# Kernel optimization log

Measured on AMD Instinct MI355X. Metric: run time of the kernel, lower is better.

Reference implementation:

```python
import jax, jax.numpy as jnp
import numpy as np

N_NODES = 100000
N_EDGES = 1600000
D_IN = 128
D_OUT = 256


def setup_inputs() -> dict:
    key = jax.random.key(0)
    k1, k2, k3 = jax.random.split(key, 3)
    H = jax.random.normal(k1, (N_NODES, D_IN), dtype=jnp.float32)
    edge_index = jax.random.randint(k2, (2, N_EDGES), 0, N_NODES, dtype=jnp.int64)
    # kaiming_normal_ on (in, out): fan computed over dim 1 -> std = sqrt(2/out)
    W = jax.random.normal(k3, (D_IN, D_OUT), dtype=jnp.float32) * np.sqrt(2.0 / D_OUT)
    return {"H": H, "edge_index": edge_index, "W": W}


def reference(H, edge_index, W):
    src, dst = edge_index[0], edge_index[1]
    # gather source node features per edge, scatter-add into destination nodes
    msgs = H[src]  # [E, D_IN]
    new_H = jax.ops.segment_sum(msgs, dst, num_segments=H.shape[0])  # [N, D_IN]
    out = H + new_H
    out = out @ W  # [N, D_OUT]
    return jax.nn.relu(out)
```

## Files before the change

### kernel.cpp

```cpp
#include <hip/hip_runtime.h>

#define N_NODES 100000
#define N_EDGES 1600000
#define D_IN    128
#define D_OUT   256
#define NB_SCAN ((N_NODES + 255) / 256)
#define BLK_ROWS 64
#define N_TILES  ((N_NODES + BLK_ROWS - 1) / BLK_ROWS)
#define X_ROWS   (N_TILES * BLK_ROWS)

#define NBUCK      98
#define BCAP       20480
#define BIN_CHUNK  1024
#define BIN_BLOCKS ((N_EDGES + BIN_CHUNK - 1) / BIN_CHUNK)

typedef __attribute__((ext_vector_type(8))) short short8v;
typedef __attribute__((ext_vector_type(4))) float f32x4;

__device__ __forceinline__ unsigned bf16_rn(float f) {
    unsigned u = __float_as_uint(f);
    return (u + 0x7FFFu + ((u >> 16) & 1u)) >> 16;
}
__device__ __forceinline__ unsigned pack2_bf16(float a, float b) {
    return bf16_rn(a) | (bf16_rn(b) << 16);
}

__global__ void detect_idx64_kernel(const int* __restrict__ edge32,
                                    int* __restrict__ flag,
                                    int* __restrict__ balloc) {
    const int t = threadIdx.x;
    if (t < 128) balloc[t] = 0;
    if (t == 0 && blockIdx.x == 0) {
        int is64 = 1;
        for (int i = 1; i < 32; i += 2) {
            if (edge32[i] != 0) { is64 = 0; break; }
        }
        *flag = is64;
    }
}

__device__ __forceinline__ int load_dst(const void* edge_raw, int is64, int e) {
    if (is64) return (int)((const long long*)edge_raw)[(long long)N_EDGES + e];
    return ((const int*)edge_raw)[N_EDGES + e];
}
__device__ __forceinline__ int load_src(const void* edge_raw, int is64, int e) {
    if (is64) return (int)((const long long*)edge_raw)[e];
    return ((const int*)edge_raw)[e];
}

__global__ __launch_bounds__(256) void cvt_h_kernel(
        const float* __restrict__ H, unsigned* __restrict__ Hb) {
    int i = blockIdx.x * 256 + threadIdx.x;
    if (i >= N_NODES * (D_IN / 2)) return;
    const float2 h = ((const float2*)H)[i];
    Hb[i] = pack2_bf16(h.x, h.y);
}

__global__ __launch_bounds__(256) void pack_w_kernel(
        const float* __restrict__ W, unsigned short* __restrict__ Wp) {
    int t = blockIdx.x * 256 + threadIdx.x;
    if (t >= 64 * 64) return;
    const int f  = t >> 6;
    const int l  = t & 63;
    const int nb = f >> 2;
    const int ks = f & 3;
    const int col  = nb * 16 + (l & 15);
    const int krow = ks * 32 + (l >> 4) * 8;
    #pragma unroll
    for (int i = 0; i < 8; ++i)
        Wp[(size_t)t * 8 + i] = (unsigned short)bf16_rn(W[(krow + i) * D_OUT + col]);
}

__global__ __launch_bounds__(256) void bin_hist_kernel(
        const void* __restrict__ edge_raw, const int* __restrict__ flag,
        int* __restrict__ bucket_alloc, int* __restrict__ binned) {
    __shared__ int cnt[128];
    __shared__ int gbase[128];
    const int tid = threadIdx.x;
    if (tid < 128) cnt[tid] = 0;
    __syncthreads();
    const int is64 = *flag;
    const int base = blockIdx.x * BIN_CHUNK + tid;

#define EDGE_A(i)                                                             \
    int rec##i = 0, pb##i = -1;                                               \
    {                                                                         \
        const int idx = base + (i) * 256;                                     \
        if (idx < N_EDGES) {                                                  \
            const int s = load_src(edge_raw, is64, idx);                      \
            const int d = load_dst(edge_raw, is64, idx);                      \
            if ((unsigned)s < N_NODES && (unsigned)d < N_NODES) {             \
                const int b = d >> 10;                                        \
                const int pos = atomicAdd(&cnt[b], 1);                        \
                rec##i = s | ((d & 1023) << 17);                              \
                pb##i  = pos | (b << 12);                                     \
            }                                                                 \
        }                                                                     \
    }
    EDGE_A(0) EDGE_A(1) EDGE_A(2) EDGE_A(3)
#undef EDGE_A

    __syncthreads();
    if (tid < NBUCK) gbase[tid] = atomicAdd(&bucket_alloc[tid], cnt[tid]);
    __syncthreads();

#define EDGE_B(i)                                                             \
    if (pb##i >= 0) {                                                         \
        const int b = pb##i >> 12;                                            \
        const int p = gbase[b] + (pb##i & 4095);                              \
        if (p < BCAP) binned[b * BCAP + p] = rec##i;                          \
    }
    EDGE_B(0) EDGE_B(1) EDGE_B(2) EDGE_B(3)
#undef EDGE_B
}

__global__ __launch_bounds__(1024) void bucket_fill_scan_kernel(
        const int* __restrict__ bucket_alloc,
        const int* __restrict__ binned,
        int* __restrict__ row_start, int* __restrict__ csr_pack) {
    __shared__ int hist[1024];
    __shared__ int sb[128];
    const int b   = blockIdx.x;
    const int tid = threadIdx.x;
    hist[tid] = 0;
    if (tid < 128) sb[tid] = (tid < NBUCK) ? bucket_alloc[tid] : 0;
    __syncthreads();

    for (int off = 1; off < 128; off <<= 1) {
        const int u = (tid >= off && tid < 128) ? sb[tid - off] : 0;
        __syncthreads();
        if (tid < 128) sb[tid] += u;
        __syncthreads();
    }
    int cnt = bucket_alloc[b];
    const int segb = sb[b] - cnt;
    if (cnt > BCAP) cnt = BCAP;
    const int base = b * BCAP;

    for (int p = tid; p < cnt; p += 1024)
        atomicAdd(&hist[(binned[base + p] >> 17) & 1023], 1);
    __syncthreads();

    const int myc = hist[tid];
    for (int off = 1; off < 1024; off <<= 1) {
        const int u = (tid >= off) ? hist[tid - off] : 0;
        __syncthreads();
        hist[tid] += u;
        __syncthreads();
    }
    const int rs = segb + hist[tid] - myc;
    const int node = (b << 10) + tid;
    if (node <= N_NODES) row_start[node] = rs;

    hist[tid] = rs;
    __syncthreads();

    for (int p = tid; p < cnt; p += 1024) {
        const int rec = binned[base + p];
        const int dlo = (rec >> 17) & 1023;
        const int pos = atomicAdd(&hist[dlo], 1);
        csr_pack[pos] = (rec & 0x1FFFF) | ((dlo & 63) << 20);
    }
}

__global__ __launch_bounds__(256) void gather_mfma_kernel(
        const float* __restrict__ H,
        const unsigned* __restrict__ Hb,
        const int* __restrict__ row_start,
        const int* __restrict__ csr_pack,
        const unsigned short* __restrict__ Wp,
        float* __restrict__ out) {
    __shared__ unsigned Xs[64 * 64];
    __shared__ int idx_lds[4][256];

    const int g    = blockIdx.x * BLK_ROWS;
    const int wv   = threadIdx.x >> 6;
    const int lane = threadIdx.x & 63;
    const int r0   = g + wv * 16;

    if (r0 < N_NODES) {
        int r1 = r0 + 16; if (r1 > N_NODES) r1 = N_NODES;
        const int p0   = row_start[r0];
        const int pend = row_start[r1];

        for (int r = r0; r < r1; ++r) {
            if (row_start[r + 1] == row_start[r]) {
                const float2 h = ((const float2*)(H + (size_t)r * D_IN))[lane];
                const int rr = r - g;
                Xs[rr * 64 + ((((lane >> 2) ^ (rr & 7)) << 2) | (lane & 3))] =
                    pack2_bf16(h.x, h.y);
            }
        }

        int    cur = -1;
        float2 acc = make_float2(0.f, 0.f);
        float2 hs  = make_float2(0.f, 0.f);

#define FLUSH()                                                               \
        Xs[cur * 64 + ((((lane >> 2) ^ (cur & 7)) << 2) | (lane & 3))] =      \
            pack2_bf16(acc.x + hs.x, acc.y + hs.y);

#define PROC(EV, UU)                                                          \
        {                                                                     \
            const int dl = (EV) >> 20;                                        \
            const float vx = __uint_as_float((UU) << 16);                     \
            const float vy = __uint_as_float((UU) & 0xFFFF0000u);             \
            if (dl != cur) {                                                  \
                if (cur >= 0) { FLUSH(); }                                    \
                cur = dl;                                                     \
                hs  = ((const float2*)(H + (size_t)(g + dl) * D_IN))[lane];   \
                acc = make_float2(vx, vy);                                    \
            } else {                                                          \
                acc.x += vx; acc.y += vy;                                     \
            }                                                                 \
        }

        for (int p = p0; p < pend; p += 256) {
            int m = pend - p;
            if (m > 256) m = 256;
            #pragma unroll
            for (int j = 0; j < 4; ++j) {
                const int o = lane + j * 64;
                if (o < m) idx_lds[wv][o] = csr_pack[p + o];
            }
            int n = 0;
            for (; n + 8 <= m; n += 8) {
                const int e0 = idx_lds[wv][n + 0];
                const int e1 = idx_lds[wv][n + 1];
                const int e2 = idx_lds[wv][n + 2];
                const int e3 = idx_lds[wv][n + 3];
                const int e4 = idx_lds[wv][n + 4];
                const int e5 = idx_lds[wv][n + 5];
                const int e6 = idx_lds[wv][n + 6];
                const int e7 = idx_lds[wv][n + 7];
                const unsigned u0 = Hb[(size_t)(e0 & 0xFFFFF) * 64 + lane];
                const unsigned u1 = Hb[(size_t)(e1 & 0xFFFFF) * 64 + lane];
                const unsigned u2 = Hb[(size_t)(e2 & 0xFFFFF) * 64 + lane];
                const unsigned u3 = Hb[(size_t)(e3 & 0xFFFFF) * 64 + lane];
                const unsigned u4 = Hb[(size_t)(e4 & 0xFFFFF) * 64 + lane];
                const unsigned u5 = Hb[(size_t)(e5 & 0xFFFFF) * 64 + lane];
                const unsigned u6 = Hb[(size_t)(e6 & 0xFFFFF) * 64 + lane];
                const unsigned u7 = Hb[(size_t)(e7 & 0xFFFFF) * 64 + lane];
                PROC(e0, u0) PROC(e1, u1) PROC(e2, u2) PROC(e3, u3)
                PROC(e4, u4) PROC(e5, u5) PROC(e6, u6) PROC(e7, u7)
            }
            for (; n < m; ++n) {
                const int e0 = idx_lds[wv][n];
                const unsigned u = Hb[(size_t)(e0 & 0xFFFFF) * 64 + lane];
                PROC(e0, u)
            }
        }
        if (cur >= 0) { FLUSH(); }
#undef PROC
#undef FLUSH
    }
    __syncthreads();

    f32x4 acc4[4][4] = {};
    const int arow = lane & 15;
    const int agrp = lane >> 4;

    #pragma unroll
    for (int ks = 0; ks < 4; ++ks) {
        short8v a0, a1, a2, a3;
        {
            const int r = 0 * 16 + arow;
            a0 = *(const short8v*)(&Xs[r * 64 + ((ks * 4 + agrp) ^ (r & 7)) * 4]);
        }
        {
            const int r = 1 * 16 + arow;
            a1 = *(const short8v*)(&Xs[r * 64 + ((ks * 4 + agrp) ^ (r & 7)) * 4]);
        }
        {
            const int r = 2 * 16 + arow;
            a2 = *(const short8v*)(&Xs[r * 64 + ((ks * 4 + agrp) ^ (r & 7)) * 4]);
        }
        {
            const int r = 3 * 16 + arow;
            a3 = *(const short8v*)(&Xs[r * 64 + ((ks * 4 + agrp) ^ (r & 7)) * 4]);
        }
        #pragma unroll
        for (int nb = 0; nb < 4; ++nb) {
            const int f = (wv * 4 + nb) * 4 + ks;
            const short8v bf = *(const short8v*)(Wp + ((size_t)f * 64 + lane) * 8);
            acc4[0][nb] = __builtin_amdgcn_mfma_f32_16x16x32_bf16(a0, bf, acc4[0][nb], 0, 0, 0);
            acc4[1][nb] = __builtin_amdgcn_mfma_f32_16x16x32_bf16(a1, bf, acc4[1][nb], 0, 0, 0);
            acc4[2][nb] = __builtin_amdgcn_mfma_f32_16x16x32_bf16(a2, bf, acc4[2][nb], 0, 0, 0);
            acc4[3][nb] = __builtin_amdgcn_mfma_f32_16x16x32_bf16(a3, bf, acc4[3][nb], 0, 0, 0);
        }
    }

    #pragma unroll
    for (int mg = 0; mg < 4; ++mg) {
        #pragma unroll
        for (int rr = 0; rr < 4; ++rr) {
            const int row = g + mg * 16 + agrp * 4 + rr;
            if (row < N_NODES) {
                #pragma unroll
                for (int nb = 0; nb < 4; ++nb) {
                    const float v = acc4[mg][nb][rr];
                    out[(size_t)row * D_OUT + wv * 64 + nb * 16 + (lane & 15)] =
                        fmaxf(v, 0.f);
                }
            }
        }
    }
}

__global__ __launch_bounds__(256) void hist_kernel(
        const void* __restrict__ edge_raw, const int* __restrict__ flag,
        int* __restrict__ counts) {
    int e = blockIdx.x * blockDim.x + threadIdx.x;
    if (e >= N_EDGES) return;
    int dst = load_dst(edge_raw, *flag, e);
    if ((unsigned)dst < N_NODES) atomicAdd(&counts[dst], 1);
}

__global__ __launch_bounds__(256) void block_sum_kernel(
        const int* __restrict__ counts, int* __restrict__ bsum) {
    __shared__ int lds[256];
    int t = threadIdx.x;
    int i = blockIdx.x * 256 + t;
    lds[t] = (i < N_NODES) ? counts[i] : 0;
    __syncthreads();
    for (int off = 128; off > 0; off >>= 1) {
        if (t < off) lds[t] += lds[t + off];
        __syncthreads();
    }
    if (t == 0) bsum[blockIdx.x] = lds[0];
}

__global__ __launch_bounds__(512) void scan_bsum_kernel(
        int* __restrict__ bsum, int* __restrict__ row_start) {
    __shared__ int lds[512];
    int t = threadIdx.x;
    lds[t] = (t < NB_SCAN) ? bsum[t] : 0;
    __syncthreads();
    for (int off = 1; off < 512; off <<= 1) {
        int u = (t >= off) ? lds[t - off] : 0;
        __syncthreads();
        lds[t] += u;
        __syncthreads();
    }
    int excl = (t == 0) ? 0 : lds[t - 1];
    if (t < NB_SCAN) bsum[t] = excl;
    if (t == 0) row_start[N_NODES] = N_EDGES;
}

__global__ __launch_bounds__(256) void scan_counts_kernel(
        int* __restrict__ counts_cursor, const int* __restrict__ bsum,
        int* __restrict__ row_start) {
    __shared__ int lds[256];
    int t = threadIdx.x;
    int i = blockIdx.x * 256 + t;
    int c = (i < N_NODES) ? counts_cursor[i] : 0;
    lds[t] = c;
    __syncthreads();
    for (int off = 1; off < 256; off <<= 1) {
        int u = (t >= off) ? lds[t - off] : 0;
        __syncthreads();
        lds[t] += u;
        __syncthreads();
    }
    int rs = bsum[blockIdx.x] + lds[t] - c;
    if (i < N_NODES) {
        row_start[i] = rs;
        counts_cursor[i] = rs;
    }
}

__global__ __launch_bounds__(256) void fill_kernel(
        const void* __restrict__ edge_raw, const int* __restrict__ flag,
        int* __restrict__ cursor, int* __restrict__ csr_pack) {
    int e = blockIdx.x * blockDim.x + threadIdx.x;
    if (e >= N_EDGES) return;
    int is64 = *flag;
    int src = load_src(edge_raw, is64, e);
    int dst = load_dst(edge_raw, is64, e);
    if ((unsigned)dst >= N_NODES || (unsigned)src >= N_NODES) return;
    int pos = atomicAdd(&cursor[dst], 1);
    csr_pack[pos] = src | ((dst & 63) << 20);
}

__global__ __launch_bounds__(256) void fused_gather_gemm_relu_kernel(
        const float* __restrict__ H,
        const int* __restrict__ row_start,
        const int* __restrict__ csr_pack,
        const float* __restrict__ Wm,
        float* __restrict__ out) {
    __shared__ float Xs[BLK_ROWS][D_IN];
    __shared__ int idx_lds[4][64];

    const int g    = blockIdx.x * BLK_ROWS;
    const int tid  = threadIdx.x;
    const int wv   = tid >> 6;
    const int lane = tid & 63;

    {
        const int kidx = tid & 31;
        const int rg   = tid >> 5;
        #pragma unroll
        for (int j = 0; j < 8; ++j) {
            const int r = rg + j * 8;
            const int row = g + r;
            float4 x = make_float4(0.f, 0.f, 0.f, 0.f);
            if (row < N_NODES)
                x = *reinterpret_cast<const float4*>(H + (size_t)row * D_IN + kidx * 4);
            *reinterpret_cast<float4*>(&Xs[r][kidx * 4]) = x;
        }
    }
    __syncthreads();

    {
        const int seg_beg = row_start[g];
        const int rend    = (g + BLK_ROWS < N_NODES) ? (g + BLK_ROWS) : N_NODES;
        const int seg_end = row_start[rend];
        const int len     = seg_end - seg_beg;
        const int clen    = (len + 3) >> 2;
        const int cbeg    = seg_beg + wv * clen;
        int cend          = cbeg + clen;
        if (cend > seg_end) cend = seg_end;

        const int c2 = lane * 2;
        int   cur = -1;
        float2 acc = make_float2(0.f, 0.f);

#define PROCF(EV, VV)                                                         \
        {                                                                     \
            const int dl = (EV) >> 20;                                        \
            if (dl != cur) {                                                  \
                if (cur >= 0) {                                               \
                    atomicAdd(&Xs[cur][c2],     acc.x);                       \
                    atomicAdd(&Xs[cur][c2 + 1], acc.y);                       \
                }                                                             \
                cur = dl;                                                     \
                acc = (VV);                                                   \
            } else {                                                          \
                acc.x += (VV).x; acc.y += (VV).y;                             \
            }                                                                 \
        }

        for (int base = cbeg; base < cend; base += 64) {
            int m = cend - base;
            if (m > 64) m = 64;
            if (lane < m) idx_lds[wv][lane] = csr_pack[base + lane];
            int n = 0;
            for (; n + 8 <= m; n += 8) {
                const int e0 = idx_lds[wv][n + 0];
                const int e1 = idx_lds[wv][n + 1];
                const int e2 = idx_lds[wv][n + 2];
                const int e3 = idx_lds[wv][n + 3];
                const int e4 = idx_lds[wv][n + 4];
                const int e5 = idx_lds[wv][n + 5];
                const int e6 = idx_lds[wv][n + 6];
                const int e7 = idx_lds[wv][n + 7];
                const float2 v0 = ((const float2*)(H + (size_t)(e0 & 0xFFFFF) * D_IN))[lane];
                const float2 v1 = ((const float2*)(H + (size_t)(e1 & 0xFFFFF) * D_IN))[lane];
                const float2 v2 = ((const float2*)(H + (size_t)(e2 & 0xFFFFF) * D_IN))[lane];
                const float2 v3 = ((const float2*)(H + (size_t)(e3 & 0xFFFFF) * D_IN))[lane];
                const float2 v4 = ((const float2*)(H + (size_t)(e4 & 0xFFFFF) * D_IN))[lane];
                const float2 v5 = ((const float2*)(H + (size_t)(e5 & 0xFFFFF) * D_IN))[lane];
                const float2 v6 = ((const float2*)(H + (size_t)(e6 & 0xFFFFF) * D_IN))[lane];
                const float2 v7 = ((const float2*)(H + (size_t)(e7 & 0xFFFFF) * D_IN))[lane];
                PROCF(e0, v0) PROCF(e1, v1) PROCF(e2, v2) PROCF(e3, v3)
                PROCF(e4, v4) PROCF(e5, v5) PROCF(e6, v6) PROCF(e7, v7)
            }
            for (; n < m; ++n) {
                const int e0 = idx_lds[wv][n];
                const float2 v = ((const float2*)(H + (size_t)(e0 & 0xFFFFF) * D_IN))[lane];
                PROCF(e0, v)
            }
        }
        if (cur >= 0) {
            atomicAdd(&Xs[cur][c2],     acc.x);
            atomicAdd(&Xs[cur][c2 + 1], acc.y);
        }
#undef PROCF
    }
    __syncthreads();

    const int ty = tid >> 6;
    const int tx = tid & 63;

    float accv[16][4];
    #pragma unroll
    for (int r = 0; r < 16; ++r)
        #pragma unroll
        for (int j = 0; j < 4; ++j) accv[r][j] = 0.f;

    const float* Wp2 = Wm + tx * 4;

    #pragma unroll 2
    for (int k = 0; k < D_IN; k += 4) {
        const float4 w0 = *reinterpret_cast<const float4*>(Wp2 + (k + 0) * D_OUT);
        const float4 w1 = *reinterpret_cast<const float4*>(Wp2 + (k + 1) * D_OUT);
        const float4 w2 = *reinterpret_cast<const float4*>(Wp2 + (k + 2) * D_OUT);
        const float4 w3 = *reinterpret_cast<const float4*>(Wp2 + (k + 3) * D_OUT);
        #pragma unroll
        for (int r = 0; r < 16; ++r) {
            const float4 x = *reinterpret_cast<const float4*>(&Xs[ty * 16 + r][k]);
            accv[r][0] = fmaf(x.x, w0.x, accv[r][0]);
            accv[r][0] = fmaf(x.y, w1.x, accv[r][0]);
            accv[r][0] = fmaf(x.z, w2.x, accv[r][0]);
            accv[r][0] = fmaf(x.w, w3.x, accv[r][0]);
            accv[r][1] = fmaf(x.x, w0.y, accv[r][1]);
            accv[r][1] = fmaf(x.y, w1.y, accv[r][1]);
            accv[r][1] = fmaf(x.z, w2.y, accv[r][1]);
            accv[r][1] = fmaf(x.w, w3.y, accv[r][1]);
            accv[r][2] = fmaf(x.x, w0.z, accv[r][2]);
            accv[r][2] = fmaf(x.y, w1.z, accv[r][2]);
            accv[r][2] = fmaf(x.z, w2.z, accv[r][2]);
            accv[r][2] = fmaf(x.w, w3.z, accv[r][2]);
            accv[r][3] = fmaf(x.x, w0.w, accv[r][3]);
            accv[r][3] = fmaf(x.y, w1.w, accv[r][3]);
            accv[r][3] = fmaf(x.z, w2.w, accv[r][3]);
            accv[r][3] = fmaf(x.w, w3.w, accv[r][3]);
        }
    }

    #pragma unroll
    for (int r = 0; r < 16; ++r) {
        const int row = g + ty * 16 + r;
        if (row < N_NODES) {
            float4 o;
            o.x = fmaxf(accv[r][0], 0.f);
            o.y = fmaxf(accv[r][1], 0.f);
            o.z = fmaxf(accv[r][2], 0.f);
            o.w = fmaxf(accv[r][3], 0.f);
            *reinterpret_cast<float4*>(out + (size_t)row * D_OUT + tx * 4) = o;
        }
    }
}

extern "C" void kernel_launch(void* const* d_in, const int* in_sizes, int n_in,
                              void* d_out, int out_size, void* d_ws, size_t ws_size,
                              hipStream_t stream) {
    const float* H    = (const float*)d_in[0];
    const void*  edge = d_in[1];
    const float* Wm   = (const float*)d_in[2];
    float* out = (float*)d_out;

    const size_t off_rs    = 0;
    const size_t off_cur   = ((size_t)(N_NODES + 1) * 4 + 15) & ~(size_t)15;
    const size_t off_alloc = off_cur + (size_t)N_NODES * 4;
    const size_t off_csr   = off_alloc + 512;
    const size_t off_bsum  = off_csr + (size_t)N_EDGES * 4;
    const size_t off_flag  = off_bsum + (((size_t)NB_SCAN * 4 + 15) & ~(size_t)15);
    const size_t off_wp    = (off_flag + 16 + 255) & ~(size_t)255;
    const size_t off_X     = (off_wp + 64 * 64 * 16 + 255) & ~(size_t)255;
    const size_t need_mid  = off_X + (size_t)X_ROWS * 64 * sizeof(unsigned);
    const size_t off_Hb    = (need_mid + 255) & ~(size_t)255;
    const size_t need_full = off_Hb + (size_t)N_NODES * (D_IN / 2) * sizeof(unsigned);
    const size_t off_bin   = (need_full + 255) & ~(size_t)255;
    const size_t need_sort = off_bin + (size_t)NBUCK * BCAP * 4;

    int* row_start = (int*)((char*)d_ws + off_rs);
    int* cursor    = (int*)((char*)d_ws + off_cur);
    int* balloc    = (int*)((char*)d_ws + off_alloc);
    int* csr_pack  = (int*)((char*)d_ws + off_csr);
    int* bsum      = (int*)((char*)d_ws + off_bsum);
    int* flag      = (int*)((char*)d_ws + off_flag);
    unsigned short* Wp = (unsigned short*)((char*)d_ws + off_wp);
    unsigned* Hb   = (unsigned*)((char*)d_ws + off_Hb);
    int* binned    = (int*)((char*)d_ws + off_bin);

    detect_idx64_kernel<<<1, 128, 0, stream>>>((const int*)edge, flag, balloc);

    const int edge_blocks = (N_EDGES + 255) / 256;

    if (ws_size >= need_sort) {
        pack_w_kernel<<<16, 256, 0, stream>>>(Wm, Wp);
        cvt_h_kernel<<<(N_NODES * (D_IN / 2) + 255) / 256, 256, 0, stream>>>(H, Hb);
        bin_hist_kernel<<<BIN_BLOCKS, 256, 0, stream>>>(edge, flag, balloc, binned);
        bucket_fill_scan_kernel<<<NBUCK, 1024, 0, stream>>>(
            balloc, binned, row_start, csr_pack);
        gather_mfma_kernel<<<N_TILES, 256, 0, stream>>>(
            H, Hb, row_start, csr_pack, Wp, out);
    } else {
        hipMemsetAsync(cursor, 0, (size_t)N_NODES * 4 + 512, stream);
        hist_kernel<<<edge_blocks, 256, 0, stream>>>(edge, flag, cursor);
        block_sum_kernel<<<NB_SCAN, 256, 0, stream>>>(cursor, bsum);
        scan_bsum_kernel<<<1, 512, 0, stream>>>(bsum, row_start);
        scan_counts_kernel<<<NB_SCAN, 256, 0, stream>>>(cursor, bsum, row_start);
        fill_kernel<<<edge_blocks, 256, 0, stream>>>(edge, flag, cursor, csr_pack);
        fused_gather_gemm_relu_kernel<<<N_TILES, 256, 0, stream>>>(
            H, row_start, csr_pack, Wm, out);
    }
}
```

Baseline: 206.3 us.

## Merge prep kernels and split gather from MFMA GEMM via bf16 buffer

Three preprocessing kernels (W packing, H bf16 conversion, edge binning) are merged into one launch dispatched by block index. The fused gather+GEMM kernel is split into a gather kernel with 32-row blocks (8 rows per wave) that writes bf16 aggregated rows to a global buffer with nontemporal stores. A separate GEMM kernel then loads 64-row tiles into swizzled LDS and preloads the W fragments into registers. This raises parallelism for the irregular gather and separates it from the MFMA phase, at the cost of an extra global round-trip of about 25 MB and one more kernel launch.

```diff
diff --git a/kernel.cpp b/kernel.cpp
--- a/kernel.cpp
+++ b/kernel.cpp
@@ -13,6 +13,11 @@
 #define BCAP       20480
 #define BIN_CHUNK  1024
 #define BIN_BLOCKS ((N_EDGES + BIN_CHUNK - 1) / BIN_CHUNK)
+#define CVT_BLOCKS ((N_NODES * (D_IN / 2) + 255) / 256)
+#define PACK_BLOCKS 16
+
+#define GBLK_ROWS  32
+#define G_TILES    ((N_NODES + GBLK_ROWS - 1) / GBLK_ROWS)
 
 typedef __attribute__((ext_vector_type(8))) short short8v;
 typedef __attribute__((ext_vector_type(4))) float f32x4;
@@ -48,39 +53,43 @@
     return ((const int*)edge_raw)[e];
 }
 
-__global__ __launch_bounds__(256) void cvt_h_kernel(
-        const float* __restrict__ H, unsigned* __restrict__ Hb) {
-    int i = blockIdx.x * 256 + threadIdx.x;
-    if (i >= N_NODES * (D_IN / 2)) return;
-    const float2 h = ((const float2*)H)[i];
-    Hb[i] = pack2_bf16(h.x, h.y);
-}
-
-__global__ __launch_bounds__(256) void pack_w_kernel(
-        const float* __restrict__ W, unsigned short* __restrict__ Wp) {
-    int t = blockIdx.x * 256 + threadIdx.x;
-    if (t >= 64 * 64) return;
-    const int f  = t >> 6;
-    const int l  = t & 63;
-    const int nb = f >> 2;
-    const int ks = f & 3;
-    const int col  = nb * 16 + (l & 15);
-    const int krow = ks * 32 + (l >> 4) * 8;
-    #pragma unroll
-    for (int i = 0; i < 8; ++i)
-        Wp[(size_t)t * 8 + i] = (unsigned short)bf16_rn(W[(krow + i) * D_OUT + col]);
-}
-
-__global__ __launch_bounds__(256) void bin_hist_kernel(
+__global__ __launch_bounds__(256) void prep_kernel(
+        const float* __restrict__ W, unsigned short* __restrict__ Wp,
+        const float* __restrict__ H, unsigned* __restrict__ Hb,
         const void* __restrict__ edge_raw, const int* __restrict__ flag,
         int* __restrict__ bucket_alloc, int* __restrict__ binned) {
+    const int blk = blockIdx.x;
+    const int tid = threadIdx.x;
+
+    if (blk < PACK_BLOCKS) {
+        const int t = blk * 256 + tid;
+        const int f  = t >> 6;
+        const int l  = t & 63;
+        const int nb = f >> 2;
+        const int ks = f & 3;
+        const int col  = nb * 16 + (l & 15);
+        const int krow = ks * 32 + (l >> 4) * 8;
+        #pragma unroll
+        for (int i = 0; i < 8; ++i)
+            Wp[(size_t)t * 8 + i] =
+                (unsigned short)bf16_rn(W[(krow + i) * D_OUT + col]);
+        return;
+    }
+    if (blk < PACK_BLOCKS + CVT_BLOCKS) {
+        const int i = (blk - PACK_BLOCKS) * 256 + tid;
+        if (i < N_NODES * (D_IN / 2)) {
+            const float2 h = ((const float2*)H)[i];
+            Hb[i] = pack2_bf16(h.x, h.y);
+        }
+        return;
+    }
+
     __shared__ int cnt[128];
     __shared__ int gbase[128];
-    const int tid = threadIdx.x;
     if (tid < 128) cnt[tid] = 0;
     __syncthreads();
     const int is64 = *flag;
-    const int base = blockIdx.x * BIN_CHUNK + tid;
+    const int base = (blk - PACK_BLOCKS - CVT_BLOCKS) * BIN_CHUNK + tid;
 
 #define EDGE_A(i)                                                             \
     int rec##i = 0, pb##i = -1;                                               \
@@ -163,102 +172,131 @@
     }
 }
 
-__global__ __launch_bounds__(256) void gather_mfma_kernel(
+__global__ __launch_bounds__(256) void gather_bf16_kernel(
         const float* __restrict__ H,
         const unsigned* __restrict__ Hb,
         const int* __restrict__ row_start,
         const int* __restrict__ csr_pack,
+        unsigned* __restrict__ Xg) {
+    __shared__ int idx_lds[4][256];
+
+    const int gb   = blockIdx.x * GBLK_ROWS;
+    const int tile = (gb >> 6) << 6;
+    const int wv   = threadIdx.x >> 6;
+    const int lane = threadIdx.x & 63;
+    const int r0   = gb + wv * 8;
+    if (r0 >= N_NODES) return;
+    int r1 = r0 + 8; if (r1 > N_NODES) r1 = N_NODES;
+
+    const int p0   = row_start[r0];
+    const int pend = row_start[r1];
+
+    for (int r = r0; r < r1; ++r) {
+        if (row_start[r + 1] == row_start[r]) {
+            const float2 h = ((const float2*)(H + (size_t)r * D_IN))[lane];
+            __builtin_nontemporal_store(pack2_bf16(h.x, h.y),
+                                        &Xg[(size_t)r * 64 + lane]);
+        }
+    }
+
+    int    cur = -1;
+    float2 acc = make_float2(0.f, 0.f);
+    float2 hs  = make_float2(0.f, 0.f);
+
+#define FLUSH()                                                               \
+    __builtin_nontemporal_store(pack2_bf16(acc.x + hs.x, acc.y + hs.y),       \
+                                &Xg[(size_t)(tile + cur) * 64 + lane]);
+
+#define PROC(EV, UU)                                                          \
+    {                                                                         \
+        const int dl = (EV) >> 20;                                            \
+        const float vx = __uint_as_float((UU) << 16);                         \
+        const float vy = __uint_as_float((UU) & 0xFFFF0000u);                 \
+        if (dl != cur) {                                                      \
+            if (cur >= 0) { FLUSH(); }                                        \
+            cur = dl;                                                         \
+            hs  = ((const float2*)(H + (size_t)(tile + dl) * D_IN))[lane];    \
+            acc = make_float2(vx, vy);                                        \
+        } else {                                                              \
+            acc.x += vx; acc.y += vy;                                         \
+        }                                                                     \
+    }
+
+    for (int p = p0; p < pend; p += 256) {
+        int m = pend - p;
+        if (m > 256) m = 256;
+        #pragma unroll
+        for (int j = 0; j < 4; ++j) {
+            const int o = lane + j * 64;
+            if (o < m) idx_lds[wv][o] = csr_pack[p + o];
+        }
+        int n = 0;
+        for (; n + 8 <= m; n += 8) {
+            const int e0 = idx_lds[wv][n + 0];
+            const int e1 = idx_lds[wv][n + 1];
+            const int e2 = idx_lds[wv][n + 2];
+            const int e3 = idx_lds[wv][n + 3];
+            const int e4 = idx_lds[wv][n + 4];
+            const int e5 = idx_lds[wv][n + 5];
+            const int e6 = idx_lds[wv][n + 6];
+            const int e7 = idx_lds[wv][n + 7];
+            const unsigned u0 = Hb[(size_t)(e0 & 0xFFFFF) * 64 + lane];
+            const unsigned u1 = Hb[(size_t)(e1 & 0xFFFFF) * 64 + lane];
+            const unsigned u2 = Hb[(size_t)(e2 & 0xFFFFF) * 64 + lane];
+            const unsigned u3 = Hb[(size_t)(e3 & 0xFFFFF) * 64 + lane];
+            const unsigned u4 = Hb[(size_t)(e4 & 0xFFFFF) * 64 + lane];
+            const unsigned u5 = Hb[(size_t)(e5 & 0xFFFFF) * 64 + lane];
+            const unsigned u6 = Hb[(size_t)(e6 & 0xFFFFF) * 64 + lane];
+            const unsigned u7 = Hb[(size_t)(e7 & 0xFFFFF) * 64 + lane];
+            PROC(e0, u0) PROC(e1, u1) PROC(e2, u2) PROC(e3, u3)
+            PROC(e4, u4) PROC(e5, u5) PROC(e6, u6) PROC(e7, u7)
+        }
+        for (; n < m; ++n) {
+            const int e0 = idx_lds[wv][n];
+            const unsigned u = Hb[(size_t)(e0 & 0xFFFFF) * 64 + lane];
+            PROC(e0, u)
+        }
+    }
+    if (cur >= 0) { FLUSH(); }
+#undef PROC
+#undef FLUSH
+}
+
+__global__ __launch_bounds__(256) void gemm_mfma_kernel(
+        const unsigned* __restrict__ Xg,
         const unsigned short* __restrict__ Wp,
         float* __restrict__ out) {
     __shared__ unsigned Xs[64 * 64];
-    __shared__ int idx_lds[4][256];
-
-    const int g    = blockIdx.x * BLK_ROWS;
-    const int wv   = threadIdx.x >> 6;
-    const int lane = threadIdx.x & 63;
-    const int r0   = g + wv * 16;
-
-    if (r0 < N_NODES) {
-        int r1 = r0 + 16; if (r1 > N_NODES) r1 = N_NODES;
-        const int p0   = row_start[r0];
-        const int pend = row_start[r1];
-
-        for (int r = r0; r < r1; ++r) {
-            if (row_start[r + 1] == row_start[r]) {
-                const float2 h = ((const float2*)(H + (size_t)r * D_IN))[lane];
-                const int rr = r - g;
-                Xs[rr * 64 + ((((lane >> 2) ^ (rr & 7)) << 2) | (lane & 3))] =
-                    pack2_bf16(h.x, h.y);
-            }
-        }
-
-        int    cur = -1;
-        float2 acc = make_float2(0.f, 0.f);
-        float2 hs  = make_float2(0.f, 0.f);
-
-#define FLUSH()                                                               \
-        Xs[cur * 64 + ((((lane >> 2) ^ (cur & 7)) << 2) | (lane & 3))] =      \
-            pack2_bf16(acc.x + hs.x, acc.y + hs.y);
-
-#define PROC(EV, UU)                                                          \
-        {                                                                     \
-            const int dl = (EV) >> 20;                                        \
-            const float vx = __uint_as_float((UU) << 16);                     \
-            const float vy = __uint_as_float((UU) & 0xFFFF0000u);             \
-            if (dl != cur) {                                                  \
-                if (cur >= 0) { FLUSH(); }                                    \
-                cur = dl;                                                     \
-                hs  = ((const float2*)(H + (size_t)(g + dl) * D_IN))[lane];   \
-                acc = make_float2(vx, vy);                                    \
-            } else {                                                          \
-                acc.x += vx; acc.y += vy;                                     \
-            }                                                                 \
-        }
-
-        for (int p = p0; p < pend; p += 256) {
-            int m = pend - p;
-            if (m > 256) m = 256;
-            #pragma unroll
-            for (int j = 0; j < 4; ++j) {
-                const int o = lane + j * 64;
-                if (o < m) idx_lds[wv][o] = csr_pack[p + o];
-            }
-            int n = 0;
-            for (; n + 8 <= m; n += 8) {
-                const int e0 = idx_lds[wv][n + 0];
-                const int e1 = idx_lds[wv][n + 1];
-                const int e2 = idx_lds[wv][n + 2];
-                const int e3 = idx_lds[wv][n + 3];
-                const int e4 = idx_lds[wv][n + 4];
-                const int e5 = idx_lds[wv][n + 5];
-                const int e6 = idx_lds[wv][n + 6];
-                const int e7 = idx_lds[wv][n + 7];
-                const unsigned u0 = Hb[(size_t)(e0 & 0xFFFFF) * 64 + lane];
-                const unsigned u1 = Hb[(size_t)(e1 & 0xFFFFF) * 64 + lane];
-                const unsigned u2 = Hb[(size_t)(e2 & 0xFFFFF) * 64 + lane];
-                const unsigned u3 = Hb[(size_t)(e3 & 0xFFFFF) * 64 + lane];
-                const unsigned u4 = Hb[(size_t)(e4 & 0xFFFFF) * 64 + lane];
-                const unsigned u5 = Hb[(size_t)(e5 & 0xFFFFF) * 64 + lane];
-                const unsigned u6 = Hb[(size_t)(e6 & 0xFFFFF) * 64 + lane];
-                const unsigned u7 = Hb[(size_t)(e7 & 0xFFFFF) * 64 + lane];
-                PROC(e0, u0) PROC(e1, u1) PROC(e2, u2) PROC(e3, u3)
-                PROC(e4, u4) PROC(e5, u5) PROC(e6, u6) PROC(e7, u7)
-            }
-            for (; n < m; ++n) {
-                const int e0 = idx_lds[wv][n];
-                const unsigned u = Hb[(size_t)(e0 & 0xFFFFF) * 64 + lane];
-                PROC(e0, u)
-            }
-        }
-        if (cur >= 0) { FLUSH(); }
-#undef PROC
-#undef FLUSH
-    }
-    __syncthreads();
-
-    f32x4 acc4[4][4] = {};
-    const int arow = lane & 15;
-    const int agrp = lane >> 4;
+
+    const int tid = threadIdx.x;
+    const int w   = tid >> 6;
+    const int l   = tid & 63;
+    const int g   = blockIdx.x * BLK_ROWS;
+
+    #pragma unroll
+    for (int j = 0; j < 4; ++j) {
+        const int flat = j * 256 + tid;
+        const int r   = flat >> 4;
+        const int c16 = flat & 15;
+        const uint4 v = *(const uint4*)(Xg + (size_t)(g + r) * 64 + c16 * 4);
+        const int pc = c16 ^ (r & 7);
+        *(uint4*)(&Xs[r * 64 + pc * 4]) = v;
+    }
+
+    short8v bfr[4][4];
+    #pragma unroll
+    for (int nb = 0; nb < 4; ++nb)
+        #pragma unroll
+        for (int ks = 0; ks < 4; ++ks) {
+            const int f = (w * 4 + nb) * 4 + ks;
+            bfr[nb][ks] = *(const short8v*)(Wp + ((size_t)f * 64 + l) * 8);
+        }
+
+    __syncthreads();
+
+    f32x4 acc[4][4] = {};
+    const int arow = l & 15;
+    const int agrp = l >> 4;
 
     #pragma unroll
     for (int ks = 0; ks < 4; ++ks) {
@@ -281,12 +319,10 @@
         }
         #pragma unroll
         for (int nb = 0; nb < 4; ++nb) {
-            const int f = (wv * 4 + nb) * 4 + ks;
-            const short8v bf = *(const short8v*)(Wp + ((size_t)f * 64 + lane) * 8);
-            acc4[0][nb] = __builtin_amdgcn_mfma_f32_16x16x32_bf16(a0, bf, acc4[0][nb], 0, 0, 0);
-            acc4[1][nb] = __builtin_amdgcn_mfma_f32_16x16x32_bf16(a1, bf, acc4[1][nb], 0, 0, 0);
-            acc4[2][nb] = __builtin_amdgcn_mfma_f32_16x16x32_bf16(a2, bf, acc4[2][nb], 0, 0, 0);
-            acc4[3][nb] = __builtin_amdgcn_mfma_f32_16x16x32_bf16(a3, bf, acc4[3][nb], 0, 0, 0);
+            acc[0][nb] = __builtin_amdgcn_mfma_f32_16x16x32_bf16(a0, bfr[nb][ks], acc[0][nb], 0, 0, 0);
+            acc[1][nb] = __builtin_amdgcn_mfma_f32_16x16x32_bf16(a1, bfr[nb][ks], acc[1][nb], 0, 0, 0);
+            acc[2][nb] = __builtin_amdgcn_mfma_f32_16x16x32_bf16(a2, bfr[nb][ks], acc[2][nb], 0, 0, 0);
+            acc[3][nb] = __builtin_amdgcn_mfma_f32_16x16x32_bf16(a3, bfr[nb][ks], acc[3][nb], 0, 0, 0);
         }
     }
 
@@ -298,8 +334,8 @@
             if (row < N_NODES) {
                 #pragma unroll
                 for (int nb = 0; nb < 4; ++nb) {
-                    const float v = acc4[mg][nb][rr];
-                    out[(size_t)row * D_OUT + wv * 64 + nb * 16 + (lane & 15)] =
+                    const float v = acc[mg][nb][rr];
+                    out[(size_t)row * D_OUT + w * 64 + nb * 16 + (l & 15)] =
                         fmaxf(v, 0.f);
                 }
             }
@@ -561,6 +597,7 @@
     int* bsum      = (int*)((char*)d_ws + off_bsum);
     int* flag      = (int*)((char*)d_ws + off_flag);
     unsigned short* Wp = (unsigned short*)((char*)d_ws + off_wp);
+    unsigned* Xg   = (unsigned*)((char*)d_ws + off_X);
     unsigned* Hb   = (unsigned*)((char*)d_ws + off_Hb);
     int* binned    = (int*)((char*)d_ws + off_bin);
 
@@ -569,13 +606,13 @@
     const int edge_blocks = (N_EDGES + 255) / 256;
 
     if (ws_size >= need_sort) {
-        pack_w_kernel<<<16, 256, 0, stream>>>(Wm, Wp);
-        cvt_h_kernel<<<(N_NODES * (D_IN / 2) + 255) / 256, 256, 0, stream>>>(H, Hb);
-        bin_hist_kernel<<<BIN_BLOCKS, 256, 0, stream>>>(edge, flag, balloc, binned);
+        prep_kernel<<<PACK_BLOCKS + CVT_BLOCKS + BIN_BLOCKS, 256, 0, stream>>>(
+            Wm, Wp, H, Hb, edge, flag, balloc, binned);
         bucket_fill_scan_kernel<<<NBUCK, 1024, 0, stream>>>(
             balloc, binned, row_start, csr_pack);
-        gather_mfma_kernel<<<N_TILES, 256, 0, stream>>>(
-            H, Hb, row_start, csr_pack, Wp, out);
+        gather_bf16_kernel<<<G_TILES, 256, 0, stream>>>(
+            H, Hb, row_start, csr_pack, Xg);
+        gemm_mfma_kernel<<<N_TILES, 256, 0, stream>>>(Xg, Wp, out);
     } else {
         hipMemsetAsync(cursor, 0, (size_t)N_NODES * 4 + 512, stream);
         hist_kernel<<<edge_blocks, 256, 0, stream>>>(edge, flag, cursor);
```

Measured after the change: 179.4 us. -13.1%, faster.
